# Performance work log

Measured on AMD Instinct MI355X. Metric: run time of the kernel, lower is better.

## Reference

```python
import jax, jax.numpy as jnp
import numpy as np

B = 2048
WIDTH = 128      # channel width == 1D signal length after unsqueeze
MODES = 16       # retained Fourier modes
INPUT_DIM = 100
T_DIM = 28
U_DIM = 64
NFREQ = WIDTH // 2 + 1


def setup_inputs() -> dict:
    key = jax.random.key(0)
    ks = jax.random.split(key, 32)
    rn = lambda k, s: jax.random.normal(k, s, jnp.float32)
    un = lambda k, s: jax.random.uniform(k, s, jnp.float32)
    sc_in0 = 1.0 / (1 * WIDTH)        # SpectralConv scale for conv0 (in=1)
    sc_in = 1.0 / (WIDTH * WIDTH)     # for conv1..3
    inp = {
        "X1": rn(ks[0], (B, INPUT_DIM + T_DIM)),
        "fc0_w": rn(ks[1], (WIDTH, INPUT_DIM + T_DIM)) * 0.02,
        "fc0_b": jnp.zeros((WIDTH,), jnp.float32),
        # spectral weights: torch.rand(..., cfloat) -> uniform real & imag in [0,1), scaled
        "sc0_wr": un(ks[2], (1, WIDTH, MODES)) * sc_in0,
        "sc0_wi": un(ks[3], (1, WIDTH, MODES)) * sc_in0,
        "sc1_wr": un(ks[4], (WIDTH, WIDTH, MODES)) * sc_in,
        "sc1_wi": un(ks[5], (WIDTH, WIDTH, MODES)) * sc_in,
        "sc2_wr": un(ks[6], (WIDTH, WIDTH, MODES)) * sc_in,
        "sc2_wi": un(ks[7], (WIDTH, WIDTH, MODES)) * sc_in,
        "sc3_wr": un(ks[8], (WIDTH, WIDTH, MODES)) * sc_in,
        "sc3_wi": un(ks[9], (WIDTH, WIDTH, MODES)) * sc_in,
        # pointwise (kernel-size-1) Conv1d weights as [out, in] + bias
        "w0_w": rn(ks[10], (WIDTH, 1)) * 0.02,
        "w0_b": jnp.zeros((WIDTH,), jnp.float32),
        "w1_w": rn(ks[11], (WIDTH, WIDTH)) * 0.02,
        "w1_b": jnp.zeros((WIDTH,), jnp.float32),
        "w2_w": rn(ks[12], (WIDTH, WIDTH)) * 0.02,
        "w2_b": jnp.zeros((WIDTH,), jnp.float32),
        "w3_w": rn(ks[13], (WIDTH, WIDTH)) * 0.02,
        "w3_b": jnp.zeros((WIDTH,), jnp.float32),
        "fc1_w": rn(ks[14], (WIDTH, WIDTH * WIDTH)) * 0.01,
        "fc1_b": jnp.zeros((WIDTH,), jnp.float32),
        "fc2_w": rn(ks[15], (U_DIM, WIDTH)) * 0.02,
        "fc2_b": jnp.zeros((U_DIM,), jnp.float32),
    }
    return inp


def _spectral_conv(x, wr, wi):
    # x: [B, Cin, L]; wr/wi: [Cin, Cout, MODES]
    L = x.shape[-1]
    xf = jnp.fft.rfft(x)                                   # [B, Cin, L//2+1] complex
    w = wr + 1j * wi
    of = jnp.einsum('bim,iom->bom', xf[:, :, :MODES], w)   # [B, Cout, MODES]
    of = jnp.pad(of, ((0, 0), (0, 0), (0, L // 2 + 1 - MODES)))
    return jnp.fft.irfft(of, n=L)                          # [B, Cout, L] real


def _pointwise(x, w, b):
    # kernel-size-1 Conv1d: x [B, Cin, L], w [Cout, Cin], b [Cout]
    return jnp.einsum('bil,oi->bol', x, w) + b[None, :, None]


def _gelu(x):
    return jax.nn.gelu(x, approximate=False)  # torch F.gelu default (erf)


def reference(X1, fc0_w, fc0_b, sc0_wr, sc0_wi, sc1_wr, sc1_wi, sc2_wr, sc2_wi,
              sc3_wr, sc3_wi, w0_w, w0_b, w1_w, w1_b, w2_w, w2_b, w3_w, w3_b,
              fc1_w, fc1_b, fc2_w, fc2_b):
    # fc0: lift [B, input_dim+t_dim] -> [B, width]
    x = X1 @ fc0_w.T + fc0_b
    x = x[:, None, :]  # [B, 1, WIDTH]
    x = _gelu(_spectral_conv(x, sc0_wr, sc0_wi) + _pointwise(x, w0_w, w0_b))
    x = _gelu(_spectral_conv(x, sc1_wr, sc1_wi) + _pointwise(x, w1_w, w1_b))
    x = _gelu(_spectral_conv(x, sc2_wr, sc2_wi) + _pointwise(x, w2_w, w2_b))
    x = _spectral_conv(x, sc3_wr, sc3_wi) + _pointwise(x, w3_w, w3_b)
    x = x.reshape(x.shape[0], -1)              # [B, WIDTH*WIDTH]
    x = _gelu(x @ fc1_w.T + fc1_b)
    x = x @ fc2_w.T + fc2_b                    # [B, U_DIM]
    return jnp.squeeze(x)
```

## Files before the change

### kernel.cpp

```cpp
#include <hip/hip_runtime.h>
#include <math.h>

#define PI_D 3.14159265358979323846

#define OFF_TW   0u
#define OFF_X0   4096u
#define OFF_PWT  OFF_X0
#define OFF_TWT  (OFF_X0 + 49152u)
#define OFF_WT   (OFF_X0 + 262144u)
#define OFF_XFR  (OFF_WT + 1572864u)
#define OFF_XFI  (OFF_XFR + 4194304u)
#define OFF_OFR  (OFF_XFI + 4194304u)
#define OFF_OFI  (OFF_OFR + 4194304u)
#define OFF_A    (OFF_OFI + 4194304u)
#define OFF_HP   OFF_XFR

__device__ __forceinline__ float gelu_f(float x) {
    return 0.5f * x * (1.0f + erff(x * 0.7071067811865476f));
}

__device__ __forceinline__ int swzc(int c4) { return 4 * (c4 ^ ((c4 >> 3) & 3)); }

__global__ void k_setup(float* ws) {
    int id = blockIdx.x * 256 + threadIdx.x;
    if (id < 4096) {
        int l = id >> 5, c = id & 31, m = c & 15;
        double ang = (PI_D / 64.0) * (double)((m * l) & 127);
        double v = (c < 16) ? cos(ang) : -sin(ang);
        ws[OFF_TW + id] = (float)v;
    }
}

__global__ void k_transpose(const float* w1r, const float* w1i,
                            const float* w2r, const float* w2i,
                            const float* w3r, const float* w3i, float* ws) {
    int id = blockIdx.x * 256 + threadIdx.x;
    int lay = id >> 18;
    int rem = id & 262143;
    int m = rem >> 14, i = (rem >> 7) & 127, o = rem & 127;
    const float* sr = (lay == 0) ? w1r : (lay == 1) ? w2r : w3r;
    const float* si = (lay == 0) ? w1i : (lay == 1) ? w2i : w3i;
    int src = (i * 128 + o) * 16 + m;
    ws[OFF_WT + (unsigned)lay * 524288u + rem] = sr[src];
    ws[OFF_WT + (unsigned)lay * 524288u + 262144u + rem] = si[src];
}

__global__ void k_prep2(const float* w1w, const float* w2w, const float* w3w, float* ws) {
    int id = blockIdx.x * 256 + threadIdx.x;
    if (id < 49152) {
        int lay = id >> 14, rem = id & 16383;
        int i = rem >> 7, o = rem & 127;
        const float* w = (lay == 0) ? w1w : (lay == 1) ? w2w : w3w;
        ws[OFF_PWT + id] = w[o * 128 + i];
    } else if (id < 53248) {
        int id2 = id - 49152;
        int c = id2 >> 7, l = id2 & 127;
        ws[OFF_TWT + c * 128 + l] = ws[OFF_TW + l * 32 + c];
    }
}

__global__ __launch_bounds__(256) void k_fc0(const float* X1, const float* w, const float* bias, float* ws) {
    __shared__ float xs[16][128];
    __shared__ float wsm[128][129];
    int t = threadIdx.x;
    int b0 = blockIdx.x * 16;
#pragma unroll
    for (int q = 0; q < 8; ++q) {
        int idx = q * 256 + t;
        xs[idx >> 7][idx & 127] = X1[b0 * 128 + idx];
    }
#pragma unroll
    for (int q = 0; q < 64; ++q) {
        int idx = q * 256 + t;
        wsm[idx >> 7][idx & 127] = w[idx];
    }
    __syncthreads();
    int c = t & 127, bh = t >> 7;
    float* x0 = ws + OFF_X0;
    for (int j = 0; j < 8; ++j) {
        int b = bh * 8 + j;
        float acc = bias[c];
#pragma unroll 8
        for (int k = 0; k < 128; ++k) acc += xs[b][k] * wsm[c][k];
        x0[(b0 + b) * 128 + c] = acc;
    }
}

__global__ __launch_bounds__(256) void k_layer0(const float* w0r, const float* w0i,
                                                const float* w0w, const float* w0b, float* ws) {
    __shared__ float x0s[128];
    __shared__ float tws[128][33];
    __shared__ float xrs[16], xis[16];
    __shared__ __align__(16) float ors[2048];
    __shared__ __align__(16) float ois[2048];
    int t = threadIdx.x, b = blockIdx.x;
    const float* tw = ws + OFF_TW;
    const float* x0 = ws + OFF_X0;
    if (t < 128) x0s[t] = x0[b * 128 + t];
#pragma unroll
    for (int q = 0; q < 16; ++q) {
        int idx = q * 256 + t;
        tws[idx >> 5][idx & 31] = tw[idx];
    }
    __syncthreads();
    if (t < 32) {
        float acc = 0.f;
        for (int l = 0; l < 128; ++l) acc += x0s[l] * tws[l][t];
        if (t < 16) xrs[t] = acc; else xis[t - 16] = acc;
    }
    __syncthreads();
#pragma unroll
    for (int q = 0; q < 8; ++q) {
        int idx = q * 256 + t;
        int m = idx & 15;
        float wr = w0r[idx], wi = w0i[idx];
        float sc = (m == 0) ? (1.f / 128.f) : (2.f / 128.f);
        float xr = xrs[m], xi = xis[m];
        ors[idx] = (xr * wr - xi * wi) * sc;
        ois[idx] = (xr * wi + xi * wr) * sc;
    }
    __syncthreads();
    int l = t & 127, og = t >> 7;
    float tvc[16], tvs[16];
#pragma unroll
    for (int m = 0; m < 16; ++m) { tvc[m] = tws[l][m]; tvs[m] = tws[l][16 + m]; }
    float xl = x0s[l];
    float* A = ws + OFF_A + b * 16384;
    const float4* or4 = (const float4*)ors;
    const float4* oi4 = (const float4*)ois;
    for (int oj = 0; oj < 64; ++oj) {
        int o = og * 64 + oj;
        float acc = xl * w0w[o] + w0b[o];
#pragma unroll
        for (int q = 0; q < 4; ++q) {
            float4 r4 = or4[o * 4 + q];
            float4 i4 = oi4[o * 4 + q];
            acc += r4.x * tvc[4 * q + 0] + i4.x * tvs[4 * q + 0];
            acc += r4.y * tvc[4 * q + 1] + i4.y * tvs[4 * q + 1];
            acc += r4.z * tvc[4 * q + 2] + i4.z * tvs[4 * q + 2];
            acc += r4.w * tvc[4 * q + 3] + i4.w * tvs[4 * q + 3];
        }
        A[o * 128 + l] = gelu_f(acc);
    }
}

__global__ __launch_bounds__(256) void k_dft(float* ws) {
    __shared__ float as_[16][260];
    __shared__ float tws_[16][32];
    int t = threadIdx.x;
    int row0 = blockIdx.x * 256;
    const float* A = ws + OFF_A;
    const float* tw = ws + OFF_TW;
    int tr = t >> 3, tc = t & 7;
    float acc[8][4];
#pragma unroll
    for (int j = 0; j < 8; ++j)
#pragma unroll
        for (int cc = 0; cc < 4; ++cc) acc[j][cc] = 0.f;
    int col0 = swzc(2 * tr), col1 = swzc(2 * tr + 1);
    for (int kc = 0; kc < 8; ++kc) {
        int k0 = kc * 16;
        if (kc) __syncthreads();
#pragma unroll
        for (int q = 0; q < 4; ++q) {
            int idx = q * 256 + t;
            int r = idx >> 2, kq = idx & 3;
            float4 v = *(const float4*)&A[(row0 + r) * 128 + k0 + 4 * kq];
            int sc = swzc(r >> 2) + (r & 3);
            as_[4 * kq + 0][sc] = v.x; as_[4 * kq + 1][sc] = v.y;
            as_[4 * kq + 2][sc] = v.z; as_[4 * kq + 3][sc] = v.w;
        }
#pragma unroll
        for (int q = 0; q < 2; ++q) {
            int idx = q * 256 + t;
            tws_[idx >> 5][idx & 31] = tw[(k0 + (idx >> 5)) * 32 + (idx & 31)];
        }
        __syncthreads();
#pragma unroll 8
        for (int kk = 0; kk < 16; ++kk) {
            float4 a0 = *(const float4*)&as_[kk][col0];
            float4 a1 = *(const float4*)&as_[kk][col1];
            float4 t0 = *(const float4*)&tws_[kk][tc * 4];
            float av[8] = {a0.x,a0.y,a0.z,a0.w,a1.x,a1.y,a1.z,a1.w};
            float tv[4] = {t0.x,t0.y,t0.z,t0.w};
#pragma unroll
            for (int j = 0; j < 8; ++j)
#pragma unroll
                for (int cc = 0; cc < 4; ++cc) acc[j][cc] += av[j] * tv[cc];
        }
    }
    float* xfr = ws + OFF_XFR;
    float* xfi = ws + OFF_XFI;
#pragma unroll
    for (int cc = 0; cc < 4; ++cc) {
        int c = tc * 4 + cc;
        float* dst = (c < 16) ? (xfr + c * 262144) : (xfi + (c - 16) * 262144);
        float4 v0 = make_float4(acc[0][cc], acc[1][cc], acc[2][cc], acc[3][cc]);
        float4 v1 = make_float4(acc[4][cc], acc[5][cc], acc[6][cc], acc[7][cc]);
        *(float4*)&dst[row0 + tr * 8] = v0;
        *(float4*)&dst[row0 + tr * 8 + 4] = v1;
    }
}

__global__ __launch_bounds__(256) void k_modemix(int lay, float* ws) {
    __shared__ float xr_s[16 * 36], xi_s[16 * 36];
    __shared__ float wr_s[16 * 132], wi_s[16 * 132];
    int t = threadIdx.x;
    int b0 = blockIdx.x * 32;
    int m = blockIdx.y;
    const float* xfr = ws + OFF_XFR + m * 262144;
    const float* xfi = ws + OFF_XFI + m * 262144;
    const float* wtr = ws + OFF_WT + (unsigned)lay * 524288u + m * 16384;
    const float* wti = wtr + 262144;
    int tb = t >> 5;
    int tc = t & 31;
    int sr = (t & 127) >> 2, skq = t & 3;
    float accr[4][4], acci[4][4];
#pragma unroll
    for (int jb = 0; jb < 4; ++jb)
#pragma unroll
        for (int jc = 0; jc < 4; ++jc) { accr[jb][jc] = 0.f; acci[jb][jc] = 0.f; }
    for (int kc = 0; kc < 8; ++kc) {
        int k0 = kc * 16;
        if (kc) __syncthreads();
        {
            const float* src = (t < 128) ? xfr : xfi;
            float* dst = (t < 128) ? xr_s : xi_s;
            float4 v = *(const float4*)&src[(b0 + sr) * 128 + k0 + 4 * skq];
            dst[(4 * skq + 0) * 36 + sr] = v.x;
            dst[(4 * skq + 1) * 36 + sr] = v.y;
            dst[(4 * skq + 2) * 36 + sr] = v.z;
            dst[(4 * skq + 3) * 36 + sr] = v.w;
        }
#pragma unroll
        for (int q = 0; q < 2; ++q) {
            int idx = q * 256 + t;
            int kk = idx >> 5, oq = idx & 31;
            *(float4*)&wr_s[kk * 132 + 4 * oq] = *(const float4*)&wtr[(k0 + kk) * 128 + 4 * oq];
            *(float4*)&wi_s[kk * 132 + 4 * oq] = *(const float4*)&wti[(k0 + kk) * 128 + 4 * oq];
        }
        __syncthreads();
#pragma unroll 4
        for (int kk = 0; kk < 16; ++kk) {
            float4 xr4 = *(const float4*)&xr_s[kk * 36 + tb * 4];
            float4 xi4 = *(const float4*)&xi_s[kk * 36 + tb * 4];
            float4 wr4 = *(const float4*)&wr_s[kk * 132 + 4 * tc];
            float4 wi4 = *(const float4*)&wi_s[kk * 132 + 4 * tc];
            float xrv[4] = {xr4.x, xr4.y, xr4.z, xr4.w};
            float xiv[4] = {xi4.x, xi4.y, xi4.z, xi4.w};
            float wrv[4] = {wr4.x, wr4.y, wr4.z, wr4.w};
            float wiv[4] = {wi4.x, wi4.y, wi4.z, wi4.w};
#pragma unroll
            for (int jb = 0; jb < 4; ++jb)
#pragma unroll
                for (int jc = 0; jc < 4; ++jc) {
                    accr[jb][jc] += xrv[jb] * wrv[jc] - xiv[jb] * wiv[jc];
                    acci[jb][jc] += xrv[jb] * wiv[jc] + xiv[jb] * wrv[jc];
                }
        }
    }
    float* ofr = ws + OFF_OFR + m * 262144;
    float* ofi = ws + OFF_OFI + m * 262144;
#pragma unroll
    for (int jb = 0; jb < 4; ++jb) {
        int b = b0 + tb * 4 + jb;
        *(float4*)&ofr[b * 128 + 4 * tc] = make_float4(accr[jb][0], accr[jb][1], accr[jb][2], accr[jb][3]);
        *(float4*)&ofi[b * 128 + 4 * tc] = make_float4(acci[jb][0], acci[jb][1], acci[jb][2], acci[jb][3]);
    }
}

template <int GELU>
__global__ __launch_bounds__(256) void k_layerB(const float* pwt, const float* pw_b, float* ws) {
    __shared__ float smem[8448];
    int t = threadIdx.x, b = blockIdx.x;
    float* A = ws + OFF_A + (unsigned)b * 16384u;
    const float* ofr = ws + OFF_OFR;
    const float* ofi = ws + OFF_OFI;
    const float* twt = ws + OFF_TWT;
    int ty = t >> 4, tx = t & 15;
    int col0 = swzc(2 * tx), col1 = swzc(2 * tx + 1);
    float* ofr_s = smem;
    float* ofi_s = smem + 2048;
    float* twTs  = smem + 4096;
#pragma unroll
    for (int q = 0; q < 2; ++q) {
        int idx = q * 256 + t;
        int mm = idx >> 5, oq = idx & 31;
        float sc = (mm == 0) ? (1.f / 128.f) : (2.f / 128.f);
        float4 vr = *(const float4*)&ofr[mm * 262144 + b * 128 + 4 * oq];
        float4 vi = *(const float4*)&ofi[mm * 262144 + b * 128 + 4 * oq];
        vr.x *= sc; vr.y *= sc; vr.z *= sc; vr.w *= sc;
        vi.x *= sc; vi.y *= sc; vi.z *= sc; vi.w *= sc;
        *(float4*)&ofr_s[mm * 128 + 4 * oq] = vr;
        *(float4*)&ofi_s[mm * 128 + 4 * oq] = vi;
    }
#pragma unroll
    for (int q = 0; q < 4; ++q) {
        int idx = q * 256 + t;
        int row = idx >> 5, c4 = idx & 31;
        *(float4*)&twTs[row * 132 + swzc(c4)] = *(const float4*)&twt[row * 128 + 4 * c4];
    }
    __syncthreads();
    float acc[8][8];
#pragma unroll
    for (int jo = 0; jo < 8; ++jo)
#pragma unroll
        for (int jl = 0; jl < 8; ++jl) acc[jo][jl] = 0.f;
#pragma unroll 2
    for (int m = 0; m < 16; ++m) {
        float4 or0 = *(const float4*)&ofr_s[m * 128 + ty * 8];
        float4 or1 = *(const float4*)&ofr_s[m * 128 + ty * 8 + 4];
        float4 oi0 = *(const float4*)&ofi_s[m * 128 + ty * 8];
        float4 oi1 = *(const float4*)&ofi_s[m * 128 + ty * 8 + 4];
        float4 c0 = *(const float4*)&twTs[m * 132 + col0];
        float4 c1 = *(const float4*)&twTs[m * 132 + col1];
        float4 s0 = *(const float4*)&twTs[(16 + m) * 132 + col0];
        float4 s1 = *(const float4*)&twTs[(16 + m) * 132 + col1];
        float orv[8] = {or0.x,or0.y,or0.z,or0.w,or1.x,or1.y,or1.z,or1.w};
        float oiv[8] = {oi0.x,oi0.y,oi0.z,oi0.w,oi1.x,oi1.y,oi1.z,oi1.w};
        float cv[8]  = {c0.x,c0.y,c0.z,c0.w,c1.x,c1.y,c1.z,c1.w};
        float sv[8]  = {s0.x,s0.y,s0.z,s0.w,s1.x,s1.y,s1.z,s1.w};
#pragma unroll
        for (int jo = 0; jo < 8; ++jo)
#pragma unroll
            for (int jl = 0; jl < 8; ++jl) acc[jo][jl] += orv[jo] * cv[jl] + oiv[jo] * sv[jl];
    }
    __syncthreads();
    float* as_ = smem;
    float* wsx = smem + 4224;
    for (int ch = 0; ch < 4; ++ch) {
        int i0 = ch * 32;
        if (ch) __syncthreads();
#pragma unroll
        for (int q = 0; q < 4; ++q) {
            int idx = q * 256 + t;
            int ic = idx >> 5, lq = idx & 31;
            *(float4*)&as_[ic * 132 + swzc(lq)] = *(const float4*)&A[(i0 + ic) * 128 + 4 * lq];
        }
#pragma unroll
        for (int q = 0; q < 4; ++q) {
            int idx = q * 256 + t;
            int ic = idx >> 5, oq = idx & 31;
            *(float4*)&wsx[ic * 132 + 4 * oq] = *(const float4*)&pwt[(i0 + ic) * 128 + 4 * oq];
        }
        __syncthreads();
#pragma unroll 4
        for (int ic = 0; ic < 32; ++ic) {
            float4 a0 = *(const float4*)&as_[ic * 132 + col0];
            float4 a1 = *(const float4*)&as_[ic * 132 + col1];
            float4 w0 = *(const float4*)&wsx[ic * 132 + ty * 8];
            float4 w1 = *(const float4*)&wsx[ic * 132 + ty * 8 + 4];
            float av[8] = {a0.x,a0.y,a0.z,a0.w,a1.x,a1.y,a1.z,a1.w};
            float wv[8] = {w0.x,w0.y,w0.z,w0.w,w1.x,w1.y,w1.z,w1.w};
#pragma unroll
            for (int jo = 0; jo < 8; ++jo)
#pragma unroll
                for (int jl = 0; jl < 8; ++jl) acc[jo][jl] += wv[jo] * av[jl];
        }
    }
#pragma unroll
    for (int jo = 0; jo < 8; ++jo) {
        int o = ty * 8 + jo;
        float bv = pw_b[o];
        float v[8];
#pragma unroll
        for (int jl = 0; jl < 8; ++jl) {
            float x = acc[jo][jl] + bv;
            v[jl] = GELU ? gelu_f(x) : x;
        }
        *(float4*)&A[o * 128 + tx * 8]     = make_float4(v[0], v[1], v[2], v[3]);
        *(float4*)&A[o * 128 + tx * 8 + 4] = make_float4(v[4], v[5], v[6], v[7]);
    }
}

__global__ __launch_bounds__(256) void k_fc12(const float* fc1w, float* ws) {
    __shared__ float smem[8448];
    int t = threadIdx.x;
    int b0 = blockIdx.x * 128;
    int kz = blockIdx.y;
    const float* A = ws + OFF_A;
    int tm = t >> 4, tn = t & 15;
    int ac0 = swzc(2 * tm), ac1 = swzc(2 * tm + 1);
    int wc0 = swzc(2 * tn), wc1 = swzc(2 * tn + 1);
    float acc[8][8];
#pragma unroll
    for (int jb = 0; jb < 8; ++jb)
#pragma unroll
        for (int jc = 0; jc < 8; ++jc) acc[jb][jc] = 0.f;
    for (int ks = 0; ks < 8; ++ks) {
        int k0 = kz * 256 + ks * 32;
        if (ks) __syncthreads();
#pragma unroll
        for (int q = 0; q < 4; ++q) {
            int idx = q * 256 + t;
            int r = idx >> 3, kq = idx & 7;
            float4 v = *(const float4*)&A[(b0 + r) * 16384 + k0 + 4 * kq];
            int sl = swzc(r >> 2) + (r & 3);
            smem[(4*kq+0)*132 + sl] = v.x; smem[(4*kq+1)*132 + sl] = v.y;
            smem[(4*kq+2)*132 + sl] = v.z; smem[(4*kq+3)*132 + sl] = v.w;
        }
#pragma unroll
        for (int q = 0; q < 4; ++q) {
            int idx = q * 256 + t;
            int c = idx >> 3, kq = idx & 7;
            float4 v = *(const float4*)&fc1w[c * 16384 + k0 + 4 * kq];
            int sl = swzc(c >> 2) + (c & 3);
            smem[4224 + (4*kq+0)*132 + sl] = v.x; smem[4224 + (4*kq+1)*132 + sl] = v.y;
            smem[4224 + (4*kq+2)*132 + sl] = v.z; smem[4224 + (4*kq+3)*132 + sl] = v.w;
        }
        __syncthreads();
#pragma unroll 4
        for (int kk = 0; kk < 32; ++kk) {
            float4 a0 = *(const float4*)&smem[kk * 132 + ac0];
            float4 a1 = *(const float4*)&smem[kk * 132 + ac1];
            float4 w0 = *(const float4*)&smem[4224 + kk * 132 + wc0];
            float4 w1 = *(const float4*)&smem[4224 + kk * 132 + wc1];
            float av[8] = {a0.x,a0.y,a0.z,a0.w,a1.x,a1.y,a1.z,a1.w};
            float wv[8] = {w0.x,w0.y,w0.z,w0.w,w1.x,w1.y,w1.z,w1.w};
#pragma unroll
            for (int jb = 0; jb < 8; ++jb)
#pragma unroll
                for (int jc = 0; jc < 8; ++jc) acc[jb][jc] += av[jb] * wv[jc];
        }
    }
    float* hp = ws + OFF_HP + kz * 262144;
#pragma unroll
    for (int jb = 0; jb < 8; ++jb) {
        int b = b0 + tm * 8 + jb;
        *(float4*)&hp[b * 128 + tn * 8]     = make_float4(acc[jb][0], acc[jb][1], acc[jb][2], acc[jb][3]);
        *(float4*)&hp[b * 128 + tn * 8 + 4] = make_float4(acc[jb][4], acc[jb][5], acc[jb][6], acc[jb][7]);
    }
}

__global__ __launch_bounds__(256) void k_fc2(const float* fc1b, const float* fc2w, const float* fc2b,
                                             float* ws, float* out) {
    __shared__ float hs[8][128];
    __shared__ float w2s[64][129];
    int t = threadIdx.x;
    int b0 = blockIdx.x * 8;
    const float* hp = ws + OFF_HP;
#pragma unroll
    for (int q = 0; q < 4; ++q) {
        int idx = q * 256 + t;
        int bb = idx >> 7, c = idx & 127;
        float s = fc1b[c];
#pragma unroll 8
        for (int kz = 0; kz < 64; ++kz) s += hp[kz * 262144 + (b0 + bb) * 128 + c];
        hs[bb][c] = gelu_f(s);
    }
#pragma unroll
    for (int q = 0; q < 32; ++q) {
        int idx = q * 256 + t;
        w2s[idx >> 7][idx & 127] = fc2w[idx];
    }
    __syncthreads();
#pragma unroll
    for (int q = 0; q < 2; ++q) {
        int idx = q * 256 + t;
        int bb = idx >> 6, u = idx & 63;
        float acc = fc2b[u];
#pragma unroll 8
        for (int c = 0; c < 128; ++c) acc += hs[bb][c] * w2s[u][c];
        out[(b0 + bb) * 64 + u] = acc;
    }
}

extern "C" void kernel_launch(void* const* d_in, const int* in_sizes, int n_in,
                              void* d_out, int out_size, void* d_ws, size_t ws_size,
                              hipStream_t stream) {
    const float* X1   = (const float*)d_in[0];
    const float* fc0w = (const float*)d_in[1];
    const float* fc0b = (const float*)d_in[2];
    const float* s0r  = (const float*)d_in[3];
    const float* s0i  = (const float*)d_in[4];
    const float* s1r  = (const float*)d_in[5];
    const float* s1i  = (const float*)d_in[6];
    const float* s2r  = (const float*)d_in[7];
    const float* s2i  = (const float*)d_in[8];
    const float* s3r  = (const float*)d_in[9];
    const float* s3i  = (const float*)d_in[10];
    const float* w0w  = (const float*)d_in[11];
    const float* w0b  = (const float*)d_in[12];
    const float* w1w  = (const float*)d_in[13];
    const float* w1b  = (const float*)d_in[14];
    const float* w2w  = (const float*)d_in[15];
    const float* w2b  = (const float*)d_in[16];
    const float* w3w  = (const float*)d_in[17];
    const float* w3b  = (const float*)d_in[18];
    const float* fc1w = (const float*)d_in[19];
    const float* fc1b = (const float*)d_in[20];
    const float* fc2w = (const float*)d_in[21];
    const float* fc2b = (const float*)d_in[22];
    float* ws  = (float*)d_ws;
    float* out = (float*)d_out;

    k_setup<<<dim3(16), dim3(256), 0, stream>>>(ws);
    k_transpose<<<dim3(3072), dim3(256), 0, stream>>>(s1r, s1i, s2r, s2i, s3r, s3i, ws);
    k_fc0<<<dim3(128), dim3(256), 0, stream>>>(X1, fc0w, fc0b, ws);
    k_layer0<<<dim3(2048), dim3(256), 0, stream>>>(s0r, s0i, w0w, w0b, ws);
    k_prep2<<<dim3(208), dim3(256), 0, stream>>>(w1w, w2w, w3w, ws);

    const float* pwb[3] = {w1b, w2b, w3b};
    for (int lay = 0; lay < 3; ++lay) {
        k_dft<<<dim3(1024), dim3(256), 0, stream>>>(ws);
        k_modemix<<<dim3(64, 16), dim3(256), 0, stream>>>(lay, ws);
        const float* pwt = ws + OFF_PWT + (unsigned)lay * 16384u;
        if (lay < 2)
            k_layerB<1><<<dim3(2048), dim3(256), 0, stream>>>(pwt, pwb[lay], ws);
        else
            k_layerB<0><<<dim3(2048), dim3(256), 0, stream>>>(pwt, pwb[lay], ws);
    }

    k_fc12<<<dim3(16, 64), dim3(256), 0, stream>>>(fc1w, ws);
    k_fc2<<<dim3(256), dim3(256), 0, stream>>>(fc1b, fc2w, fc2b, ws, out);
}
```

Measured before the change: 1.059 ms.

## Restructure layerB to warp-uniform output tiles with scalar-loaded weights

Folds the irfft mode scaling (1/128 or 2/128) into the precomputed twiddle table so it is applied once in setup instead of on every block load. k_layerB is retiled so each wavefront owns 32 output channels and each lane owns 2 signal positions. Spectral coefficients and pointwise weights then become wavefront-uniform and are read straight from global memory (likely as scalar loads), which removes their shared-memory staging and most syncs. Only the activation chunk is still staged in LDS. In exchange each lane reuses less data per load, and every block re-reads the weights from global or cache.

Measured after the change: 1.092 ms. +3.1%, slower.

```diff
diff --git a/kernel.cpp b/kernel.cpp
--- a/kernel.cpp
+++ b/kernel.cpp
@@ -55,7 +55,8 @@
     } else if (id < 53248) {
         int id2 = id - 49152;
         int c = id2 >> 7, l = id2 & 127;
-        ws[OFF_TWT + c * 128 + l] = ws[OFF_TW + l * 32 + c];
+        float sc = ((c & 15) == 0) ? (1.f / 128.f) : (2.f / 128.f);
+        ws[OFF_TWT + c * 128 + l] = ws[OFF_TW + l * 32 + c] * sc;
     }
 }
 
@@ -271,63 +272,36 @@
 
 template <int GELU>
 __global__ __launch_bounds__(256) void k_layerB(const float* pwt, const float* pw_b, float* ws) {
-    __shared__ float smem[8448];
+    __shared__ float As[32][128];
     int t = threadIdx.x, b = blockIdx.x;
+    int lane = t & 63;
+    int wid = __builtin_amdgcn_readfirstlane(t >> 6);
+    int o0 = wid * 32;
     float* A = ws + OFF_A + (unsigned)b * 16384u;
-    const float* ofr = ws + OFF_OFR;
-    const float* ofi = ws + OFF_OFI;
+    const float* ofrB = ws + OFF_OFR + b * 128 + o0;
+    const float* ofiB = ws + OFF_OFI + b * 128 + o0;
     const float* twt = ws + OFF_TWT;
-    int ty = t >> 4, tx = t & 15;
-    int col0 = swzc(2 * tx), col1 = swzc(2 * tx + 1);
-    float* ofr_s = smem;
-    float* ofi_s = smem + 2048;
-    float* twTs  = smem + 4096;
-#pragma unroll
-    for (int q = 0; q < 2; ++q) {
-        int idx = q * 256 + t;
-        int mm = idx >> 5, oq = idx & 31;
-        float sc = (mm == 0) ? (1.f / 128.f) : (2.f / 128.f);
-        float4 vr = *(const float4*)&ofr[mm * 262144 + b * 128 + 4 * oq];
-        float4 vi = *(const float4*)&ofi[mm * 262144 + b * 128 + 4 * oq];
-        vr.x *= sc; vr.y *= sc; vr.z *= sc; vr.w *= sc;
-        vi.x *= sc; vi.y *= sc; vi.z *= sc; vi.w *= sc;
-        *(float4*)&ofr_s[mm * 128 + 4 * oq] = vr;
-        *(float4*)&ofi_s[mm * 128 + 4 * oq] = vi;
-    }
-#pragma unroll
-    for (int q = 0; q < 4; ++q) {
-        int idx = q * 256 + t;
-        int row = idx >> 5, c4 = idx & 31;
-        *(float4*)&twTs[row * 132 + swzc(c4)] = *(const float4*)&twt[row * 128 + 4 * c4];
-    }
-    __syncthreads();
-    float acc[8][8];
-#pragma unroll
-    for (int jo = 0; jo < 8; ++jo)
-#pragma unroll
-        for (int jl = 0; jl < 8; ++jl) acc[jo][jl] = 0.f;
+    float acc[32][2];
+#pragma unroll
+    for (int jo = 0; jo < 32; ++jo) { acc[jo][0] = 0.f; acc[jo][1] = 0.f; }
 #pragma unroll 2
     for (int m = 0; m < 16; ++m) {
-        float4 or0 = *(const float4*)&ofr_s[m * 128 + ty * 8];
-        float4 or1 = *(const float4*)&ofr_s[m * 128 + ty * 8 + 4];
-        float4 oi0 = *(const float4*)&ofi_s[m * 128 + ty * 8];
-        float4 oi1 = *(const float4*)&ofi_s[m * 128 + ty * 8 + 4];
-        float4 c0 = *(const float4*)&twTs[m * 132 + col0];
-        float4 c1 = *(const float4*)&twTs[m * 132 + col1];
-        float4 s0 = *(const float4*)&twTs[(16 + m) * 132 + col0];
-        float4 s1 = *(const float4*)&twTs[(16 + m) * 132 + col1];
-        float orv[8] = {or0.x,or0.y,or0.z,or0.w,or1.x,or1.y,or1.z,or1.w};
-        float oiv[8] = {oi0.x,oi0.y,oi0.z,oi0.w,oi1.x,oi1.y,oi1.z,oi1.w};
-        float cv[8]  = {c0.x,c0.y,c0.z,c0.w,c1.x,c1.y,c1.z,c1.w};
-        float sv[8]  = {s0.x,s0.y,s0.z,s0.w,s1.x,s1.y,s1.z,s1.w};
-#pragma unroll
-        for (int jo = 0; jo < 8; ++jo)
-#pragma unroll
-            for (int jl = 0; jl < 8; ++jl) acc[jo][jl] += orv[jo] * cv[jl] + oiv[jo] * sv[jl];
-    }
-    __syncthreads();
-    float* as_ = smem;
-    float* wsx = smem + 4224;
+        float2 ct = *(const float2*)&twt[m * 128 + 2 * lane];
+        float2 st = *(const float2*)&twt[(16 + m) * 128 + 2 * lane];
+#pragma unroll
+        for (int q = 0; q < 8; ++q) {
+            float4 orv = *(const float4*)&ofrB[m * 262144 + 4 * q];
+            float4 oiv = *(const float4*)&ofiB[m * 262144 + 4 * q];
+            acc[4*q+0][0] += orv.x * ct.x + oiv.x * st.x;
+            acc[4*q+0][1] += orv.x * ct.y + oiv.x * st.y;
+            acc[4*q+1][0] += orv.y * ct.x + oiv.y * st.x;
+            acc[4*q+1][1] += orv.y * ct.y + oiv.y * st.y;
+            acc[4*q+2][0] += orv.z * ct.x + oiv.z * st.x;
+            acc[4*q+2][1] += orv.z * ct.y + oiv.z * st.y;
+            acc[4*q+3][0] += orv.w * ct.x + oiv.w * st.x;
+            acc[4*q+3][1] += orv.w * ct.y + oiv.w * st.y;
+        }
+    }
     for (int ch = 0; ch < 4; ++ch) {
         int i0 = ch * 32;
         if (ch) __syncthreads();
@@ -335,41 +309,31 @@
         for (int q = 0; q < 4; ++q) {
             int idx = q * 256 + t;
             int ic = idx >> 5, lq = idx & 31;
-            *(float4*)&as_[ic * 132 + swzc(lq)] = *(const float4*)&A[(i0 + ic) * 128 + 4 * lq];
-        }
-#pragma unroll
-        for (int q = 0; q < 4; ++q) {
-            int idx = q * 256 + t;
-            int ic = idx >> 5, oq = idx & 31;
-            *(float4*)&wsx[ic * 132 + 4 * oq] = *(const float4*)&pwt[(i0 + ic) * 128 + 4 * oq];
+            *(float4*)&As[ic][4 * lq] = *(const float4*)&A[(i0 + ic) * 128 + 4 * lq];
         }
         __syncthreads();
 #pragma unroll 4
         for (int ic = 0; ic < 32; ++ic) {
-            float4 a0 = *(const float4*)&as_[ic * 132 + col0];
-            float4 a1 = *(const float4*)&as_[ic * 132 + col1];
-            float4 w0 = *(const float4*)&wsx[ic * 132 + ty * 8];
-            float4 w1 = *(const float4*)&wsx[ic * 132 + ty * 8 + 4];
-            float av[8] = {a0.x,a0.y,a0.z,a0.w,a1.x,a1.y,a1.z,a1.w};
-            float wv[8] = {w0.x,w0.y,w0.z,w0.w,w1.x,w1.y,w1.z,w1.w};
-#pragma unroll
-            for (int jo = 0; jo < 8; ++jo)
-#pragma unroll
-                for (int jl = 0; jl < 8; ++jl) acc[jo][jl] += wv[jo] * av[jl];
-        }
-    }
-#pragma unroll
-    for (int jo = 0; jo < 8; ++jo) {
-        int o = ty * 8 + jo;
+            float2 a = *(const float2*)&As[ic][2 * lane];
+            const float* wrow = &pwt[(i0 + ic) * 128 + o0];
+#pragma unroll
+            for (int q = 0; q < 8; ++q) {
+                float4 w4 = *(const float4*)&wrow[4 * q];
+                acc[4*q+0][0] += w4.x * a.x; acc[4*q+0][1] += w4.x * a.y;
+                acc[4*q+1][0] += w4.y * a.x; acc[4*q+1][1] += w4.y * a.y;
+                acc[4*q+2][0] += w4.z * a.x; acc[4*q+2][1] += w4.z * a.y;
+                acc[4*q+3][0] += w4.w * a.x; acc[4*q+3][1] += w4.w * a.y;
+            }
+        }
+    }
+#pragma unroll
+    for (int jo = 0; jo < 32; ++jo) {
+        int o = o0 + jo;
         float bv = pw_b[o];
-        float v[8];
-#pragma unroll
-        for (int jl = 0; jl < 8; ++jl) {
-            float x = acc[jo][jl] + bv;
-            v[jl] = GELU ? gelu_f(x) : x;
-        }
-        *(float4*)&A[o * 128 + tx * 8]     = make_float4(v[0], v[1], v[2], v[3]);
-        *(float4*)&A[o * 128 + tx * 8 + 4] = make_float4(v[4], v[5], v[6], v[7]);
+        float x0 = acc[jo][0] + bv;
+        float x1 = acc[jo][1] + bv;
+        if (GELU) { x0 = gelu_f(x0); x1 = gelu_f(x1); }
+        *(float2*)&A[o * 128 + 2 * lane] = make_float2(x0, x1);
     }
 }
 
```

## Process two batch rows per layerB block with wider register tiles

Applied to the files above, without the earlier changes.

k_layerB now handles two batch samples per block, so each thread computes an 8x16 output tile instead of 8x8. This halves the grid and lets each pointwise-weight and twiddle tile loaded into shared memory serve twice as many outputs. The 1/128 and 2/128 inverse-DFT scaling moves from a per-block multiply into the precomputed twiddle table. The swizzle helper is refactored and a 64-column swizzle is added for the wider activation tile. In exchange the kernel uses more registers and shared memory, which may lower occupancy.

New measurement: 1.132 ms. 6.9% more time.

```diff
diff --git a/kernel.cpp b/kernel.cpp
--- a/kernel.cpp
+++ b/kernel.cpp
@@ -19,7 +19,8 @@
     return 0.5f * x * (1.0f + erff(x * 0.7071067811865476f));
 }
 
-__device__ __forceinline__ int swzc(int c4) { return 4 * (c4 ^ ((c4 >> 3) & 3)); }
+__device__ __forceinline__ int swzc(int c4) { return c4 ^ ((c4 >> 3) & 3); }
+__device__ __forceinline__ int swz64(int c4) { return c4 ^ ((c4 >> 3) & 7); }
 
 __global__ void k_setup(float* ws) {
     int id = blockIdx.x * 256 + threadIdx.x;
@@ -55,7 +56,8 @@
     } else if (id < 53248) {
         int id2 = id - 49152;
         int c = id2 >> 7, l = id2 & 127;
-        ws[OFF_TWT + c * 128 + l] = ws[OFF_TW + l * 32 + c];
+        float sc = ((c & 15) == 0) ? (1.f / 128.f) : (2.f / 128.f);
+        ws[OFF_TWT + c * 128 + l] = ws[OFF_TW + l * 32 + c] * sc;
     }
 }
 
@@ -157,7 +159,7 @@
     for (int j = 0; j < 8; ++j)
 #pragma unroll
         for (int cc = 0; cc < 4; ++cc) acc[j][cc] = 0.f;
-    int col0 = swzc(2 * tr), col1 = swzc(2 * tr + 1);
+    int col0 = 4 * swzc(2 * tr), col1 = 4 * swzc(2 * tr + 1);
     for (int kc = 0; kc < 8; ++kc) {
         int k0 = kc * 16;
         if (kc) __syncthreads();
@@ -166,7 +168,7 @@
             int idx = q * 256 + t;
             int r = idx >> 2, kq = idx & 3;
             float4 v = *(const float4*)&A[(row0 + r) * 128 + k0 + 4 * kq];
-            int sc = swzc(r >> 2) + (r & 3);
+            int sc = 4 * swzc(r >> 2) + (r & 3);
             as_[4 * kq + 0][sc] = v.x; as_[4 * kq + 1][sc] = v.y;
             as_[4 * kq + 2][sc] = v.z; as_[4 * kq + 3][sc] = v.w;
         }
@@ -271,105 +273,108 @@
 
 template <int GELU>
 __global__ __launch_bounds__(256) void k_layerB(const float* pwt, const float* pw_b, float* ws) {
-    __shared__ float smem[8448];
-    int t = threadIdx.x, b = blockIdx.x;
-    float* A = ws + OFF_A + (unsigned)b * 16384u;
+    __shared__ float smem[12672];
+    int t = threadIdx.x, b2 = blockIdx.x;
+    int tx = t & 15, ty = t >> 4;
+    int bb = tx >> 3;
+    int lbase = (tx & 7) * 16;
+    unsigned bA0 = OFF_A + (unsigned)(2 * b2) * 16384u;
     const float* ofr = ws + OFF_OFR;
     const float* ofi = ws + OFF_OFI;
     const float* twt = ws + OFF_TWT;
-    int ty = t >> 4, tx = t & 15;
-    int col0 = swzc(2 * tx), col1 = swzc(2 * tx + 1);
-    float* ofr_s = smem;
-    float* ofi_s = smem + 2048;
-    float* twTs  = smem + 4096;
-#pragma unroll
-    for (int q = 0; q < 2; ++q) {
-        int idx = q * 256 + t;
-        int mm = idx >> 5, oq = idx & 31;
-        float sc = (mm == 0) ? (1.f / 128.f) : (2.f / 128.f);
-        float4 vr = *(const float4*)&ofr[mm * 262144 + b * 128 + 4 * oq];
-        float4 vi = *(const float4*)&ofi[mm * 262144 + b * 128 + 4 * oq];
-        vr.x *= sc; vr.y *= sc; vr.z *= sc; vr.w *= sc;
-        vi.x *= sc; vi.y *= sc; vi.z *= sc; vi.w *= sc;
-        *(float4*)&ofr_s[mm * 128 + 4 * oq] = vr;
-        *(float4*)&ofi_s[mm * 128 + 4 * oq] = vi;
+#pragma unroll
+    for (int q = 0; q < 8; ++q) {
+        int idx = q * 256 + t;
+        int half = idx >> 10;
+        int rem = idx & 1023;
+        int sbb = rem >> 9, mm = (rem >> 5) & 15, oq = rem & 31;
+        const float* src = half ? ofi : ofr;
+        float4 v = *(const float4*)&src[mm * 262144 + (2 * b2 + sbb) * 128 + 4 * oq];
+        *(float4*)&smem[half * 4096 + sbb * 2048 + mm * 128 + 4 * oq] = v;
     }
 #pragma unroll
     for (int q = 0; q < 4; ++q) {
         int idx = q * 256 + t;
         int row = idx >> 5, c4 = idx & 31;
-        *(float4*)&twTs[row * 132 + swzc(c4)] = *(const float4*)&twt[row * 128 + 4 * c4];
-    }
-    __syncthreads();
-    float acc[8][8];
+        *(float4*)&smem[8192 + row * 132 + 4 * swzc(c4)] = *(const float4*)&twt[row * 128 + 4 * c4];
+    }
+    __syncthreads();
+    float acc[8][16];
 #pragma unroll
     for (int jo = 0; jo < 8; ++jo)
 #pragma unroll
-        for (int jl = 0; jl < 8; ++jl) acc[jo][jl] = 0.f;
-#pragma unroll 2
+        for (int jl = 0; jl < 16; ++jl) acc[jo][jl] = 0.f;
+    int tcol[4];
+#pragma unroll
+    for (int j = 0; j < 4; ++j) tcol[j] = 4 * swzc((tx & 7) * 4 + j);
     for (int m = 0; m < 16; ++m) {
-        float4 or0 = *(const float4*)&ofr_s[m * 128 + ty * 8];
-        float4 or1 = *(const float4*)&ofr_s[m * 128 + ty * 8 + 4];
-        float4 oi0 = *(const float4*)&ofi_s[m * 128 + ty * 8];
-        float4 oi1 = *(const float4*)&ofi_s[m * 128 + ty * 8 + 4];
-        float4 c0 = *(const float4*)&twTs[m * 132 + col0];
-        float4 c1 = *(const float4*)&twTs[m * 132 + col1];
-        float4 s0 = *(const float4*)&twTs[(16 + m) * 132 + col0];
-        float4 s1 = *(const float4*)&twTs[(16 + m) * 132 + col1];
+        float4 or0 = *(const float4*)&smem[bb * 2048 + m * 128 + ty * 8];
+        float4 or1 = *(const float4*)&smem[bb * 2048 + m * 128 + ty * 8 + 4];
+        float4 oi0 = *(const float4*)&smem[4096 + bb * 2048 + m * 128 + ty * 8];
+        float4 oi1 = *(const float4*)&smem[4096 + bb * 2048 + m * 128 + ty * 8 + 4];
+        float ct[16], st[16];
+#pragma unroll
+        for (int j = 0; j < 4; ++j) {
+            *(float4*)&ct[4 * j] = *(const float4*)&smem[8192 + m * 132 + tcol[j]];
+            *(float4*)&st[4 * j] = *(const float4*)&smem[8192 + (16 + m) * 132 + tcol[j]];
+        }
         float orv[8] = {or0.x,or0.y,or0.z,or0.w,or1.x,or1.y,or1.z,or1.w};
         float oiv[8] = {oi0.x,oi0.y,oi0.z,oi0.w,oi1.x,oi1.y,oi1.z,oi1.w};
-        float cv[8]  = {c0.x,c0.y,c0.z,c0.w,c1.x,c1.y,c1.z,c1.w};
-        float sv[8]  = {s0.x,s0.y,s0.z,s0.w,s1.x,s1.y,s1.z,s1.w};
 #pragma unroll
         for (int jo = 0; jo < 8; ++jo)
 #pragma unroll
-            for (int jl = 0; jl < 8; ++jl) acc[jo][jl] += orv[jo] * cv[jl] + oiv[jo] * sv[jl];
-    }
-    __syncthreads();
-    float* as_ = smem;
-    float* wsx = smem + 4224;
+            for (int jl = 0; jl < 16; ++jl) acc[jo][jl] += orv[jo] * ct[jl] + oiv[jo] * st[jl];
+    }
+    __syncthreads();
+    int aCol[4];
+#pragma unroll
+    for (int j = 0; j < 4; ++j) aCol[j] = 4 * swz64(4 * tx + j);
     for (int ch = 0; ch < 4; ++ch) {
         int i0 = ch * 32;
         if (ch) __syncthreads();
 #pragma unroll
+        for (int q = 0; q < 8; ++q) {
+            int idx = q * 256 + t;
+            int ic = idx >> 6, c4 = idx & 63;
+            float4 v = *(const float4*)&ws[bA0 + (unsigned)((c4 >> 5) * 16384) + (unsigned)((i0 + ic) * 128) + (unsigned)(4 * (c4 & 31))];
+            *(float4*)&smem[ic * 264 + 4 * swz64(c4)] = v;
+        }
+#pragma unroll
         for (int q = 0; q < 4; ++q) {
             int idx = q * 256 + t;
-            int ic = idx >> 5, lq = idx & 31;
-            *(float4*)&as_[ic * 132 + swzc(lq)] = *(const float4*)&A[(i0 + ic) * 128 + 4 * lq];
-        }
-#pragma unroll
-        for (int q = 0; q < 4; ++q) {
-            int idx = q * 256 + t;
             int ic = idx >> 5, oq = idx & 31;
-            *(float4*)&wsx[ic * 132 + 4 * oq] = *(const float4*)&pwt[(i0 + ic) * 128 + 4 * oq];
+            *(float4*)&smem[8448 + ic * 132 + 4 * oq] = *(const float4*)&pwt[(i0 + ic) * 128 + 4 * oq];
         }
         __syncthreads();
-#pragma unroll 4
+#pragma unroll 2
         for (int ic = 0; ic < 32; ++ic) {
-            float4 a0 = *(const float4*)&as_[ic * 132 + col0];
-            float4 a1 = *(const float4*)&as_[ic * 132 + col1];
-            float4 w0 = *(const float4*)&wsx[ic * 132 + ty * 8];
-            float4 w1 = *(const float4*)&wsx[ic * 132 + ty * 8 + 4];
-            float av[8] = {a0.x,a0.y,a0.z,a0.w,a1.x,a1.y,a1.z,a1.w};
+            float a[16];
+#pragma unroll
+            for (int j = 0; j < 4; ++j)
+                *(float4*)&a[4 * j] = *(const float4*)&smem[ic * 264 + aCol[j]];
+            float4 w0 = *(const float4*)&smem[8448 + ic * 132 + ty * 8];
+            float4 w1 = *(const float4*)&smem[8448 + ic * 132 + ty * 8 + 4];
             float wv[8] = {w0.x,w0.y,w0.z,w0.w,w1.x,w1.y,w1.z,w1.w};
 #pragma unroll
             for (int jo = 0; jo < 8; ++jo)
 #pragma unroll
-                for (int jl = 0; jl < 8; ++jl) acc[jo][jl] += wv[jo] * av[jl];
+                for (int jl = 0; jl < 16; ++jl) acc[jo][jl] += wv[jo] * a[jl];
         }
     }
 #pragma unroll
     for (int jo = 0; jo < 8; ++jo) {
         int o = ty * 8 + jo;
         float bv = pw_b[o];
-        float v[8];
-#pragma unroll
-        for (int jl = 0; jl < 8; ++jl) {
+        float v[16];
+#pragma unroll
+        for (int jl = 0; jl < 16; ++jl) {
             float x = acc[jo][jl] + bv;
             v[jl] = GELU ? gelu_f(x) : x;
         }
-        *(float4*)&A[o * 128 + tx * 8]     = make_float4(v[0], v[1], v[2], v[3]);
-        *(float4*)&A[o * 128 + tx * 8 + 4] = make_float4(v[4], v[5], v[6], v[7]);
+        float* dst = ws + bA0 + (unsigned)(bb * 16384) + (unsigned)(o * 128 + lbase);
+#pragma unroll
+        for (int j = 0; j < 4; ++j)
+            *(float4*)&dst[4 * j] = make_float4(v[4*j], v[4*j+1], v[4*j+2], v[4*j+3]);
     }
 }
 
@@ -380,8 +385,8 @@
     int kz = blockIdx.y;
     const float* A = ws + OFF_A;
     int tm = t >> 4, tn = t & 15;
-    int ac0 = swzc(2 * tm), ac1 = swzc(2 * tm + 1);
-    int wc0 = swzc(2 * tn), wc1 = swzc(2 * tn + 1);
+    int ac0 = 4 * swzc(2 * tm), ac1 = 4 * swzc(2 * tm + 1);
+    int wc0 = 4 * swzc(2 * tn), wc1 = 4 * swzc(2 * tn + 1);
     float acc[8][8];
 #pragma unroll
     for (int jb = 0; jb < 8; ++jb)
@@ -395,7 +400,7 @@
             int idx = q * 256 + t;
             int r = idx >> 3, kq = idx & 7;
             float4 v = *(const float4*)&A[(b0 + r) * 16384 + k0 + 4 * kq];
-            int sl = swzc(r >> 2) + (r & 3);
+            int sl = 4 * swzc(r >> 2) + (r & 3);
             smem[(4*kq+0)*132 + sl] = v.x; smem[(4*kq+1)*132 + sl] = v.y;
             smem[(4*kq+2)*132 + sl] = v.z; smem[(4*kq+3)*132 + sl] = v.w;
         }
@@ -404,7 +409,7 @@
             int idx = q * 256 + t;
             int c = idx >> 3, kq = idx & 7;
             float4 v = *(const float4*)&fc1w[c * 16384 + k0 + 4 * kq];
-            int sl = swzc(c >> 2) + (c & 3);
+            int sl = 4 * swzc(c >> 2) + (c & 3);
             smem[4224 + (4*kq+0)*132 + sl] = v.x; smem[4224 + (4*kq+1)*132 + sl] = v.y;
             smem[4224 + (4*kq+2)*132 + sl] = v.z; smem[4224 + (4*kq+3)*132 + sl] = v.w;
         }
@@ -506,9 +511,9 @@
         k_modemix<<<dim3(64, 16), dim3(256), 0, stream>>>(lay, ws);
         const float* pwt = ws + OFF_PWT + (unsigned)lay * 16384u;
         if (lay < 2)
-            k_layerB<1><<<dim3(2048), dim3(256), 0, stream>>>(pwt, pwb[lay], ws);
+            k_layerB<1><<<dim3(1024), dim3(256), 0, stream>>>(pwt, pwb[lay], ws);
         else
-            k_layerB<0><<<dim3(2048), dim3(256), 0, stream>>>(pwt, pwb[lay], ws);
+            k_layerB<0><<<dim3(1024), dim3(256), 0, stream>>>(pwt, pwb[lay], ws);
     }
 
     k_fc12<<<dim3(16, 64), dim3(256), 0, stream>>>(fc1w, ws);
```
